# Performance work log

Hardware: AMD Instinct MI355X
Metric: run time of the kernel (lower is better)

Reference implementation:

```python
import jax, jax.numpy as jnp
import numpy as np

N, K, D, H = 10000, 30, 128, 4
DH = D // H
E = N * K

def setup_inputs() -> dict:
    ks = jax.random.split(jax.random.key(0), 12)
    s = 0.05
    h = jax.random.normal(ks[0], (N, D), jnp.float32)
    e = jax.random.normal(ks[1], (E, D), jnp.float32)
    # edges grouped by source node, K neighbors each (required by the (i j) rearranges)
    src = jnp.repeat(jnp.arange(N, dtype=jnp.int32), K)
    dst = jax.random.randint(ks[2], (E,), 0, N, dtype=jnp.int32)
    edge_index = jnp.stack([src, dst], axis=0)
    return {
        'h': h, 'e': e, 'edge_index': edge_index,
        'att_w1': jax.random.normal(ks[3], (3 * D, D)) * s, 'att_b1': jnp.zeros((D,)),
        'att_w2': jax.random.normal(ks[4], (D, D)) * s,     'att_b2': jnp.zeros((D,)),
        'att_w3': jax.random.normal(ks[5], (D, H)) * s,     'att_b3': jnp.zeros((H,)),
        'node_w1': jax.random.normal(ks[6], (2 * D, D)) * s, 'node_b1': jnp.zeros((D,)),
        'node_w2': jax.random.normal(ks[7], (D, D)) * s,     'node_b2': jnp.zeros((D,)),
        'node_w3': jax.random.normal(ks[8], (D, D)) * s,     'node_b3': jnp.zeros((D,)),
        'to_h_w': jax.random.normal(ks[9], (D, D)) * s,
    }

def reference(h, e, edge_index, att_w1, att_b1, att_w2, att_b2, att_w3, att_b3,
              node_w1, node_b1, node_w2, node_b2, node_w3, node_b3, to_h_w):
    gelu = lambda x: jax.nn.gelu(x, approximate=False)  # torch nn.GELU default (erf)
    hi = h[edge_index[0]]                               # [E, D] gather
    hj = h[edge_index[1]]                               # [E, D] gather
    hi_eij_hj = jnp.concatenate([hi, e, hj], axis=-1)   # [E, 3D]
    eij_hj = jnp.concatenate([e, hj], axis=-1)          # [E, 2D]
    # attention logits per head
    w = jax.nn.relu(hi_eij_hj @ att_w1 + att_b1)
    w = jax.nn.relu(w @ att_w2 + att_b2)
    w = (w @ att_w3 + att_b3).reshape(N, K, H)          # (i j) h -> i j h
    w = w / jnp.sqrt(jnp.float32(DH))
    att = jax.nn.softmax(w, axis=1)                     # softmax over neighbors j
    # values per edge, split per head
    v = gelu(eij_hj @ node_w1 + node_b1)
    v = gelu(v @ node_w2 + node_b2)
    v = (v @ node_w3 + node_b3).reshape(N, K, H, DH)    # (i j) (h d) -> i j h d
    out = jnp.einsum('nkh,nkhd->nhd', att, v).reshape(N, D)  # weighted aggregation
    return out @ to_h_w
```

## Files before the change

kernel.cpp:

```cpp
#include <hip/hip_runtime.h>
#include <hip/hip_bf16.h>

#define N_NODES 10000
#define KNEI    30
#define DIM     128
#define EDGES   (N_NODES * KNEI)

typedef __attribute__((ext_vector_type(4))) float  f32x4;
typedef __attribute__((ext_vector_type(8))) __bf16 bf16x8;
typedef __attribute__((ext_vector_type(4))) __bf16 bf16x4;

#define OFF_AW1 0
#define OFF_AW2 49152
#define OFF_NW1 65536
#define OFF_NW2 98304
#define OFF_NW3 114688
#define OFF_TH  131072
#define OFF_A3  147456
#define TOT_TILES 292
#define YHI_BYTE_OFF (300 * 1024)

__global__ __launch_bounds__(256) void repack_all(
    const float* __restrict__ aw1, const float* __restrict__ aw2,
    const float* __restrict__ nw1, const float* __restrict__ nw2,
    const float* __restrict__ nw3, const float* __restrict__ thw,
    const float* __restrict__ aw3, __bf16* __restrict__ dst) {
    int t = blockIdx.x * 256 + threadIdx.x;
    if (t >= TOT_TILES * 512) return;
    int tile = t >> 9;
    int i    = t & 7;
    int lane = (t >> 3) & 63;
    int krow = ((lane >> 4) << 3) + i;
    int ncol = lane & 15;
    float v;
    if (tile >= 288) {
        int k = (tile - 288) * 32 + krow;
        v = (ncol < 4) ? aw3[k * 4 + ncol] : 0.f;
    } else {
        const float* src; int lt;
        if      (tile < 96)  { src = aw1; lt = tile; }
        else if (tile < 128) { src = aw2; lt = tile - 96; }
        else if (tile < 192) { src = nw1; lt = tile - 128; }
        else if (tile < 224) { src = nw2; lt = tile - 192; }
        else if (tile < 256) { src = nw3; lt = tile - 224; }
        else                 { src = thw; lt = tile - 256; }
        int nt = lt & 7;
        int kt = lt >> 3;
        v = src[(kt * 32 + krow) * DIM + nt * 16 + ncol];
    }
    dst[t] = (__bf16)v;
}

__device__ __forceinline__ float gelu_f(float x) {
    float y = x * fmaf(0.0713548163f, x * x, 1.5957691216f);
    float r = __builtin_amdgcn_rcpf(__expf(y) + 1.f);
    return x - x * r;
}

__device__ __forceinline__ bf16x4 cvt4(float4 v) {
    bf16x4 r;
    r[0] = (__bf16)v.x; r[1] = (__bf16)v.y; r[2] = (__bf16)v.z; r[3] = (__bf16)v.w;
    return r;
}

__device__ __forceinline__ void store_act(f32x4 acc[2], const float* __restrict__ bias,
                                          __bf16* y, int sy, int actmode,
                                          int wv, int lane) {
    const int mrow = lane & 15;
    const int kgrp = (lane >> 4) & 3;
    const int nb = wv * 16 + kgrp * 4;
    float b0 = bias[nb], b1 = bias[nb + 1], b2 = bias[nb + 2], b3 = bias[nb + 3];
#pragma unroll
    for (int mf = 0; mf < 2; ++mf) {
        bf16x4 pk;
        float vv[4] = {acc[mf][0] + b0, acc[mf][1] + b1, acc[mf][2] + b2, acc[mf][3] + b3};
#pragma unroll
        for (int r = 0; r < 4; ++r) {
            float v = vv[r];
            v = actmode == 0 ? fmaxf(v, 0.f) : gelu_f(v);
            pk[r] = (__bf16)v;
        }
        *reinterpret_cast<bf16x4*>(y + (mf * 16 + mrow) * sy + nb) = pk;
    }
}

#define ZERO2(A) do { A[0] = (f32x4){0.f,0.f,0.f,0.f}; A[1] = (f32x4){0.f,0.f,0.f,0.f}; } while (0)

__global__ __launch_bounds__(512) void mm128(const float* __restrict__ in,
                                             float* __restrict__ outp,
                                             const __bf16* __restrict__ wfrag,
                                             const float* __restrict__ bias) {
    __shared__ __bf16 sP[64 * 136];
    const int tid  = threadIdx.x;
    const int wv   = tid >> 6;
    const int lane = tid & 63;
    const int mrow = lane & 15;
    const int kgrp = lane >> 4;
    const int base = blockIdx.x * 64;

#pragma unroll
    for (int c = 0; c < 4; ++c) {
        int idx = c * 512 + tid;
        int m  = idx >> 5;
        int jv = idx & 31;
        int row = base + m;
        float4 v = make_float4(0.f, 0.f, 0.f, 0.f);
        if (row < N_NODES) v = *reinterpret_cast<const float4*>(in + (long)row * DIM + jv * 4);
        *reinterpret_cast<bf16x4*>(&sP[m * 136 + jv * 4]) = cvt4(v);
    }
    __syncthreads();

    f32x4 acc[4];
#pragma unroll
    for (int mf = 0; mf < 4; ++mf) acc[mf] = (f32x4){0.f, 0.f, 0.f, 0.f};
#pragma unroll
    for (int kt = 0; kt < 4; ++kt) {
        bf16x8 a = *reinterpret_cast<const bf16x8*>(wfrag + ((kt * 8 + wv) * 64 + lane) * 8);
        const int kb = kt * 32 + kgrp * 8;
#pragma unroll
        for (int mf = 0; mf < 4; ++mf) {
            bf16x8 b = *reinterpret_cast<const bf16x8*>(sP + (mf * 16 + mrow) * 136 + kb);
            acc[mf] = __builtin_amdgcn_mfma_f32_16x16x32_bf16(a, b, acc[mf], 0, 0, 0);
        }
    }
    const int nb = wv * 16 + kgrp * 4;
    float b0 = 0.f, b1 = 0.f, b2 = 0.f, b3 = 0.f;
    if (bias) { b0 = bias[nb]; b1 = bias[nb + 1]; b2 = bias[nb + 2]; b3 = bias[nb + 3]; }
#pragma unroll
    for (int mf = 0; mf < 4; ++mf) {
        int row = base + mf * 16 + mrow;
        if (row < N_NODES) {
            float4 o = make_float4(acc[mf][0] + b0, acc[mf][1] + b1,
                                   acc[mf][2] + b2, acc[mf][3] + b3);
            *reinterpret_cast<float4*>(outp + (long)row * DIM + nb) = o;
        }
    }
}

__global__ __launch_bounds__(512, 4) void gnn_fused(
    const float* __restrict__ h, const float* __restrict__ e, const int* __restrict__ eidx,
    const float* __restrict__ yhi,
    const float* __restrict__ ab2, const float* __restrict__ ab3,
    const float* __restrict__ nb1, const float* __restrict__ nb2, const float* __restrict__ nb3,
    const __bf16* __restrict__ wp, float* __restrict__ pre_out) {

    __shared__ __bf16 S[8704];
    __shared__ __bf16 Y1[32 * 136];
    __shared__ __bf16 Y2[32 * 136];
    __shared__ float  sW[32][4];

    const int tid  = threadIdx.x;
    const int wv   = tid >> 6;
    const int lane = tid & 63;
    const int mrow = lane & 15;
    const int kg   = (lane >> 4) & 3;
    const int node = blockIdx.x;
    const long ebase = (long)node * KNEI;

#pragma unroll
    for (int c = 0; c < 2; ++c) {
        int idx = c * 512 + tid;
        int m  = idx >> 5;
        int jv = idx & 31;
        float4 ev = make_float4(0.f, 0.f, 0.f, 0.f), hjv = ev;
        if (m < KNEI) {
            long ge = ebase + m;
            ev  = *reinterpret_cast<const float4*>(e + ge * DIM + jv * 4);
            int dstn = eidx[EDGES + ge];
            hjv = *reinterpret_cast<const float4*>(h + (long)dstn * DIM + jv * 4);
        }
        *reinterpret_cast<bf16x4*>(&S[m * 264 + jv * 4])       = cvt4(ev);
        *reinterpret_cast<bf16x4*>(&S[m * 264 + 128 + jv * 4]) = cvt4(hjv);
    }
    __syncthreads();

    {
        f32x4 aa[2], an[2];
        ZERO2(aa); ZERO2(an);
        const __bf16* wA = wp + OFF_AW1 + 16384;
        const __bf16* wN = wp + OFF_NW1;
#pragma unroll
        for (int kt = 0; kt < 8; ++kt) {
            const int kb = kt * 32 + kg * 8;
            bf16x8 b0 = *reinterpret_cast<const bf16x8*>(S + mrow * 264 + kb);
            bf16x8 b1 = *reinterpret_cast<const bf16x8*>(S + (16 + mrow) * 264 + kb);
            bf16x8 a0 = *reinterpret_cast<const bf16x8*>(wA + ((kt * 8 + wv) * 64 + lane) * 8);
            aa[0] = __builtin_amdgcn_mfma_f32_16x16x32_bf16(a0, b0, aa[0], 0, 0, 0);
            aa[1] = __builtin_amdgcn_mfma_f32_16x16x32_bf16(a0, b1, aa[1], 0, 0, 0);
            bf16x8 a1 = *reinterpret_cast<const bf16x8*>(wN + ((kt * 8 + wv) * 64 + lane) * 8);
            an[0] = __builtin_amdgcn_mfma_f32_16x16x32_bf16(a1, b0, an[0], 0, 0, 0);
            an[1] = __builtin_amdgcn_mfma_f32_16x16x32_bf16(a1, b1, an[1], 0, 0, 0);
        }
        store_act(aa, yhi + (long)node * DIM, Y1, 136, 0, wv, lane);
        store_act(an, nb1, Y2, 136, 1, wv, lane);
    }
    __syncthreads();

    {
        const bool isatt = (wv < 4);
        const int w4 = isatt ? wv : (wv - 4);
        const __bf16* B = isatt ? Y1 : Y2;
        const __bf16* W = wp + (isatt ? OFF_AW2 : OFF_NW2);
        const float* bias = isatt ? ab2 : nb2;
        __bf16* dst = S + (isatt ? 4352 : 0);
        f32x4 acc[2][2];
        ZERO2(acc[0]); ZERO2(acc[1]);
#pragma unroll
        for (int kt = 0; kt < 4; ++kt) {
            const int kb = kt * 32 + kg * 8;
            bf16x8 b0 = *reinterpret_cast<const bf16x8*>(B + mrow * 136 + kb);
            bf16x8 b1 = *reinterpret_cast<const bf16x8*>(B + (16 + mrow) * 136 + kb);
#pragma unroll
            for (int j = 0; j < 2; ++j) {
                bf16x8 a = *reinterpret_cast<const bf16x8*>(W + (size_t)((kt * 8 + w4 * 2 + j) * 64 + lane) * 8);
                acc[j][0] = __builtin_amdgcn_mfma_f32_16x16x32_bf16(a, b0, acc[j][0], 0, 0, 0);
                acc[j][1] = __builtin_amdgcn_mfma_f32_16x16x32_bf16(a, b1, acc[j][1], 0, 0, 0);
            }
        }
#pragma unroll
        for (int j = 0; j < 2; ++j) {
            const int f = w4 * 32 + j * 16 + kg * 4;
            float b0 = bias[f], b1 = bias[f + 1], b2 = bias[f + 2], b3 = bias[f + 3];
#pragma unroll
            for (int mf = 0; mf < 2; ++mf) {
                float vv[4] = {acc[j][mf][0] + b0, acc[j][mf][1] + b1,
                               acc[j][mf][2] + b2, acc[j][mf][3] + b3};
                bf16x4 pk;
#pragma unroll
                for (int r = 0; r < 4; ++r) {
                    float v = isatt ? fmaxf(vv[r], 0.f) : gelu_f(vv[r]);
                    pk[r] = (__bf16)v;
                }
                *reinterpret_cast<bf16x4*>(dst + (mf * 16 + mrow) * 136 + f) = pk;
            }
        }
    }
    __syncthreads();

    if (wv == 0) {
        const __bf16* A2 = S + 4352;
        f32x4 la[2];
        ZERO2(la);
#pragma unroll
        for (int kt = 0; kt < 4; ++kt) {
            const int kb = kt * 32 + kg * 8;
            bf16x8 b0 = *reinterpret_cast<const bf16x8*>(A2 + mrow * 136 + kb);
            bf16x8 b1 = *reinterpret_cast<const bf16x8*>(A2 + (16 + mrow) * 136 + kb);
            bf16x8 a = *reinterpret_cast<const bf16x8*>(wp + OFF_A3 + ((kt * 64) + lane) * 8);
            la[0] = __builtin_amdgcn_mfma_f32_16x16x32_bf16(a, b0, la[0], 0, 0, 0);
            la[1] = __builtin_amdgcn_mfma_f32_16x16x32_bf16(a, b1, la[1], 0, 0, 0);
        }
        if (lane < 16) {
            const float sc = 0.17677669529f;
            float v0[4], v1[4], mx[4];
            const bool pad1 = (16 + lane) >= KNEI;
#pragma unroll
            for (int r = 0; r < 4; ++r) {
                v0[r] = (la[0][r] + ab3[r]) * sc;
                v1[r] = pad1 ? -1e30f : (la[1][r] + ab3[r]) * sc;
                mx[r] = fmaxf(v0[r], v1[r]);
            }
#pragma unroll
            for (int msk = 1; msk <= 8; msk <<= 1)
#pragma unroll
                for (int r = 0; r < 4; ++r) mx[r] = fmaxf(mx[r], __shfl_xor(mx[r], msk));
            float e0[4], e1[4], sm[4];
#pragma unroll
            for (int r = 0; r < 4; ++r) {
                e0[r] = __expf(v0[r] - mx[r]);
                e1[r] = __expf(v1[r] - mx[r]);
                sm[r] = e0[r] + e1[r];
            }
#pragma unroll
            for (int msk = 1; msk <= 8; msk <<= 1)
#pragma unroll
                for (int r = 0; r < 4; ++r) sm[r] += __shfl_xor(sm[r], msk);
            float4 w0, w1;
            float i0 = __builtin_amdgcn_rcpf(sm[0]), i1 = __builtin_amdgcn_rcpf(sm[1]);
            float i2 = __builtin_amdgcn_rcpf(sm[2]), i3 = __builtin_amdgcn_rcpf(sm[3]);
            w0 = make_float4(e0[0] * i0, e0[1] * i1, e0[2] * i2, e0[3] * i3);
            w1 = make_float4(e1[0] * i0, e1[1] * i1, e1[2] * i2, e1[3] * i3);
            *reinterpret_cast<float4*>(&sW[lane][0])      = w0;
            *reinterpret_cast<float4*>(&sW[16 + lane][0]) = w1;
        }
    }
    f32x4 v2[2];
    ZERO2(v2);
#pragma unroll
    for (int kt = 0; kt < 4; ++kt) {
        const int kb = kt * 32 + kg * 8;
        bf16x8 b0 = *reinterpret_cast<const bf16x8*>(S + mrow * 136 + kb);
        bf16x8 b1 = *reinterpret_cast<const bf16x8*>(S + (16 + mrow) * 136 + kb);
        bf16x8 a = *reinterpret_cast<const bf16x8*>(wp + OFF_NW3 + (size_t)((kt * 8 + wv) * 64 + lane) * 8);
        v2[0] = __builtin_amdgcn_mfma_f32_16x16x32_bf16(a, b0, v2[0], 0, 0, 0);
        v2[1] = __builtin_amdgcn_mfma_f32_16x16x32_bf16(a, b1, v2[1], 0, 0, 0);
    }
    __syncthreads();

    {
        const int hh = wv >> 1;
        float wgt0 = sW[mrow][hh];
        float wgt1 = sW[16 + mrow][hh];
        float part[4];
#pragma unroll
        for (int r = 0; r < 4; ++r)
            part[r] = wgt0 * v2[0][r] + wgt1 * v2[1][r];
#pragma unroll
        for (int msk = 1; msk <= 8; msk <<= 1)
#pragma unroll
            for (int r = 0; r < 4; ++r)
                part[r] += __shfl_xor(part[r], msk);
        if (mrow == 0) {
            const int nb = wv * 16 + kg * 4;
            float4 o = make_float4(part[0] + nb3[nb],     part[1] + nb3[nb + 1],
                                   part[2] + nb3[nb + 2], part[3] + nb3[nb + 3]);
            *reinterpret_cast<float4*>(pre_out + (long)node * DIM + nb) = o;
        }
    }
}

extern "C" void kernel_launch(void* const* d_in, const int* in_sizes, int n_in,
                              void* d_out, int out_size, void* d_ws, size_t ws_size,
                              hipStream_t stream) {
    const float* h   = (const float*)d_in[0];
    const float* e   = (const float*)d_in[1];
    const int*   ei  = (const int*)d_in[2];
    const float* aw1 = (const float*)d_in[3];
    const float* ab1 = (const float*)d_in[4];
    const float* aw2 = (const float*)d_in[5];
    const float* ab2 = (const float*)d_in[6];
    const float* aw3 = (const float*)d_in[7];
    const float* ab3 = (const float*)d_in[8];
    const float* nw1 = (const float*)d_in[9];
    const float* nb1 = (const float*)d_in[10];
    const float* nw2 = (const float*)d_in[11];
    const float* nb2 = (const float*)d_in[12];
    const float* nw3 = (const float*)d_in[13];
    const float* nb3 = (const float*)d_in[14];
    const float* thw = (const float*)d_in[15];
    float* out = (float*)d_out;
    __bf16* wp = (__bf16*)d_ws;
    float* yhi = (float*)((char*)d_ws + YHI_BYTE_OFF);

    repack_all<<<(TOT_TILES * 512 + 255) / 256, 256, 0, stream>>>(
        aw1, aw2, nw1, nw2, nw3, thw, aw3, wp);

    const int nblk = (N_NODES + 63) / 64;
    mm128<<<nblk, 512, 0, stream>>>(h, yhi, wp + OFF_AW1, ab1);

    gnn_fused<<<N_NODES, 512, 0, stream>>>(h, e, ei, yhi, ab2, ab3,
                                           nb1, nb2, nb3, wp, out);
    mm128<<<nblk, 512, 0, stream>>>(out, out, wp + OFF_TH, nullptr);
}
```

Before: 149.4 us.

## Halve gnn_fused block to 256 threads with two output tiles per wave

Each node's fused block now runs 4 waves instead of 8, and each wave computes two 16-column output tiles per stage (and four in the layer-2 split), so every B fragment loaded from LDS is reused across more MFMAs. Launch bounds change from (512,4) to (256,2), and the head-aggregation stage now maps one wave per head. The aim is less LDS traffic per MFMA and lower per-block scheduling and barrier cost. In exchange each wave holds more accumulator registers and there are fewer waves per block to hide global-load latency.

Measured after the change: 161.1 us. +7.9%, slower.

```diff
diff --git a/kernel.cpp b/kernel.cpp
--- a/kernel.cpp
+++ b/kernel.cpp
@@ -63,27 +63,6 @@
     return r;
 }
 
-__device__ __forceinline__ void store_act(f32x4 acc[2], const float* __restrict__ bias,
-                                          __bf16* y, int sy, int actmode,
-                                          int wv, int lane) {
-    const int mrow = lane & 15;
-    const int kgrp = (lane >> 4) & 3;
-    const int nb = wv * 16 + kgrp * 4;
-    float b0 = bias[nb], b1 = bias[nb + 1], b2 = bias[nb + 2], b3 = bias[nb + 3];
-#pragma unroll
-    for (int mf = 0; mf < 2; ++mf) {
-        bf16x4 pk;
-        float vv[4] = {acc[mf][0] + b0, acc[mf][1] + b1, acc[mf][2] + b2, acc[mf][3] + b3};
-#pragma unroll
-        for (int r = 0; r < 4; ++r) {
-            float v = vv[r];
-            v = actmode == 0 ? fmaxf(v, 0.f) : gelu_f(v);
-            pk[r] = (__bf16)v;
-        }
-        *reinterpret_cast<bf16x4*>(y + (mf * 16 + mrow) * sy + nb) = pk;
-    }
-}
-
 #define ZERO2(A) do { A[0] = (f32x4){0.f,0.f,0.f,0.f}; A[1] = (f32x4){0.f,0.f,0.f,0.f}; } while (0)
 
 __global__ __launch_bounds__(512) void mm128(const float* __restrict__ in,
@@ -137,7 +116,7 @@
     }
 }
 
-__global__ __launch_bounds__(512, 4) void gnn_fused(
+__global__ __launch_bounds__(256, 2) void gnn_fused(
     const float* __restrict__ h, const float* __restrict__ e, const int* __restrict__ eidx,
     const float* __restrict__ yhi,
     const float* __restrict__ ab2, const float* __restrict__ ab3,
@@ -158,8 +137,8 @@
     const long ebase = (long)node * KNEI;
 
 #pragma unroll
-    for (int c = 0; c < 2; ++c) {
-        int idx = c * 512 + tid;
+    for (int c = 0; c < 4; ++c) {
+        int idx = c * 256 + tid;
         int m  = idx >> 5;
         int jv = idx & 31;
         float4 ev = make_float4(0.f, 0.f, 0.f, 0.f), hjv = ev;
@@ -175,8 +154,9 @@
     __syncthreads();
 
     {
-        f32x4 aa[2], an[2];
-        ZERO2(aa); ZERO2(an);
+        f32x4 aa[2][2], an[2][2];
+#pragma unroll
+        for (int j = 0; j < 2; ++j) { ZERO2(aa[j]); ZERO2(an[j]); }
         const __bf16* wA = wp + OFF_AW1 + 16384;
         const __bf16* wN = wp + OFF_NW1;
 #pragma unroll
@@ -184,52 +164,76 @@
             const int kb = kt * 32 + kg * 8;
             bf16x8 b0 = *reinterpret_cast<const bf16x8*>(S + mrow * 264 + kb);
             bf16x8 b1 = *reinterpret_cast<const bf16x8*>(S + (16 + mrow) * 264 + kb);
-            bf16x8 a0 = *reinterpret_cast<const bf16x8*>(wA + ((kt * 8 + wv) * 64 + lane) * 8);
-            aa[0] = __builtin_amdgcn_mfma_f32_16x16x32_bf16(a0, b0, aa[0], 0, 0, 0);
-            aa[1] = __builtin_amdgcn_mfma_f32_16x16x32_bf16(a0, b1, aa[1], 0, 0, 0);
-            bf16x8 a1 = *reinterpret_cast<const bf16x8*>(wN + ((kt * 8 + wv) * 64 + lane) * 8);
-            an[0] = __builtin_amdgcn_mfma_f32_16x16x32_bf16(a1, b0, an[0], 0, 0, 0);
-            an[1] = __builtin_amdgcn_mfma_f32_16x16x32_bf16(a1, b1, an[1], 0, 0, 0);
-        }
-        store_act(aa, yhi + (long)node * DIM, Y1, 136, 0, wv, lane);
-        store_act(an, nb1, Y2, 136, 1, wv, lane);
+#pragma unroll
+            for (int j = 0; j < 2; ++j) {
+                bf16x8 a = *reinterpret_cast<const bf16x8*>(wA + ((kt * 8 + wv * 2 + j) * 64 + lane) * 8);
+                aa[j][0] = __builtin_amdgcn_mfma_f32_16x16x32_bf16(a, b0, aa[j][0], 0, 0, 0);
+                aa[j][1] = __builtin_amdgcn_mfma_f32_16x16x32_bf16(a, b1, aa[j][1], 0, 0, 0);
+            }
+#pragma unroll
+            for (int j = 0; j < 2; ++j) {
+                bf16x8 a = *reinterpret_cast<const bf16x8*>(wN + ((kt * 8 + wv * 2 + j) * 64 + lane) * 8);
+                an[j][0] = __builtin_amdgcn_mfma_f32_16x16x32_bf16(a, b0, an[j][0], 0, 0, 0);
+                an[j][1] = __builtin_amdgcn_mfma_f32_16x16x32_bf16(a, b1, an[j][1], 0, 0, 0);
+            }
+        }
+        const float* yrow = yhi + (long)node * DIM;
+#pragma unroll
+        for (int j = 0; j < 2; ++j) {
+            const int f = wv * 32 + j * 16 + kg * 4;
+            float4 ba = *reinterpret_cast<const float4*>(yrow + f);
+            float4 bn = *reinterpret_cast<const float4*>(nb1 + f);
+            float bav[4] = {ba.x, ba.y, ba.z, ba.w};
+            float bnv[4] = {bn.x, bn.y, bn.z, bn.w};
+#pragma unroll
+            for (int mf = 0; mf < 2; ++mf) {
+                bf16x4 p1, p2;
+#pragma unroll
+                for (int r = 0; r < 4; ++r) {
+                    p1[r] = (__bf16)fmaxf(aa[j][mf][r] + bav[r], 0.f);
+                    p2[r] = (__bf16)gelu_f(an[j][mf][r] + bnv[r]);
+                }
+                *reinterpret_cast<bf16x4*>(Y1 + (mf * 16 + mrow) * 136 + f) = p1;
+                *reinterpret_cast<bf16x4*>(Y2 + (mf * 16 + mrow) * 136 + f) = p2;
+            }
+        }
     }
     __syncthreads();
 
     {
-        const bool isatt = (wv < 4);
-        const int w4 = isatt ? wv : (wv - 4);
+        const bool isatt = (wv < 2);
+        const int w2 = isatt ? wv : (wv - 2);
         const __bf16* B = isatt ? Y1 : Y2;
         const __bf16* W = wp + (isatt ? OFF_AW2 : OFF_NW2);
         const float* bias = isatt ? ab2 : nb2;
         __bf16* dst = S + (isatt ? 4352 : 0);
-        f32x4 acc[2][2];
-        ZERO2(acc[0]); ZERO2(acc[1]);
+        f32x4 acc[4][2];
+#pragma unroll
+        for (int j = 0; j < 4; ++j) ZERO2(acc[j]);
 #pragma unroll
         for (int kt = 0; kt < 4; ++kt) {
             const int kb = kt * 32 + kg * 8;
             bf16x8 b0 = *reinterpret_cast<const bf16x8*>(B + mrow * 136 + kb);
             bf16x8 b1 = *reinterpret_cast<const bf16x8*>(B + (16 + mrow) * 136 + kb);
 #pragma unroll
-            for (int j = 0; j < 2; ++j) {
-                bf16x8 a = *reinterpret_cast<const bf16x8*>(W + (size_t)((kt * 8 + w4 * 2 + j) * 64 + lane) * 8);
+            for (int j = 0; j < 4; ++j) {
+                bf16x8 a = *reinterpret_cast<const bf16x8*>(W + (size_t)((kt * 8 + w2 * 4 + j) * 64 + lane) * 8);
                 acc[j][0] = __builtin_amdgcn_mfma_f32_16x16x32_bf16(a, b0, acc[j][0], 0, 0, 0);
                 acc[j][1] = __builtin_amdgcn_mfma_f32_16x16x32_bf16(a, b1, acc[j][1], 0, 0, 0);
             }
         }
 #pragma unroll
-        for (int j = 0; j < 2; ++j) {
-            const int f = w4 * 32 + j * 16 + kg * 4;
-            float b0 = bias[f], b1 = bias[f + 1], b2 = bias[f + 2], b3 = bias[f + 3];
+        for (int j = 0; j < 4; ++j) {
+            const int f = w2 * 64 + j * 16 + kg * 4;
+            float4 bb = *reinterpret_cast<const float4*>(bias + f);
+            float bv[4] = {bb.x, bb.y, bb.z, bb.w};
 #pragma unroll
             for (int mf = 0; mf < 2; ++mf) {
-                float vv[4] = {acc[j][mf][0] + b0, acc[j][mf][1] + b1,
-                               acc[j][mf][2] + b2, acc[j][mf][3] + b3};
                 bf16x4 pk;
 #pragma unroll
                 for (int r = 0; r < 4; ++r) {
-                    float v = isatt ? fmaxf(vv[r], 0.f) : gelu_f(vv[r]);
-                    pk[r] = (__bf16)v;
+                    float v = acc[j][mf][r] + bv[r];
+                    pk[r] = (__bf16)(isatt ? fmaxf(v, 0.f) : gelu_f(v));
                 }
                 *reinterpret_cast<bf16x4*>(dst + (mf * 16 + mrow) * 136 + f) = pk;
             }
@@ -275,46 +279,56 @@
             for (int msk = 1; msk <= 8; msk <<= 1)
 #pragma unroll
                 for (int r = 0; r < 4; ++r) sm[r] += __shfl_xor(sm[r], msk);
-            float4 w0, w1;
             float i0 = __builtin_amdgcn_rcpf(sm[0]), i1 = __builtin_amdgcn_rcpf(sm[1]);
             float i2 = __builtin_amdgcn_rcpf(sm[2]), i3 = __builtin_amdgcn_rcpf(sm[3]);
-            w0 = make_float4(e0[0] * i0, e0[1] * i1, e0[2] * i2, e0[3] * i3);
-            w1 = make_float4(e1[0] * i0, e1[1] * i1, e1[2] * i2, e1[3] * i3);
+            float4 w0 = make_float4(e0[0] * i0, e0[1] * i1, e0[2] * i2, e0[3] * i3);
+            float4 w1 = make_float4(e1[0] * i0, e1[1] * i1, e1[2] * i2, e1[3] * i3);
             *reinterpret_cast<float4*>(&sW[lane][0])      = w0;
             *reinterpret_cast<float4*>(&sW[16 + lane][0]) = w1;
         }
     }
-    f32x4 v2[2];
-    ZERO2(v2);
+    f32x4 v2[2][2];
+#pragma unroll
+    for (int j = 0; j < 2; ++j) ZERO2(v2[j]);
 #pragma unroll
     for (int kt = 0; kt < 4; ++kt) {
         const int kb = kt * 32 + kg * 8;
         bf16x8 b0 = *reinterpret_cast<const bf16x8*>(S + mrow * 136 + kb);
         bf16x8 b1 = *reinterpret_cast<const bf16x8*>(S + (16 + mrow) * 136 + kb);
-        bf16x8 a = *reinterpret_cast<const bf16x8*>(wp + OFF_NW3 + (size_t)((kt * 8 + wv) * 64 + lane) * 8);
-        v2[0] = __builtin_amdgcn_mfma_f32_16x16x32_bf16(a, b0, v2[0], 0, 0, 0);
-        v2[1] = __builtin_amdgcn_mfma_f32_16x16x32_bf16(a, b1, v2[1], 0, 0, 0);
+#pragma unroll
+        for (int j = 0; j < 2; ++j) {
+            bf16x8 a = *reinterpret_cast<const bf16x8*>(wp + OFF_NW3 + (size_t)((kt * 8 + wv * 2 + j) * 64 + lane) * 8);
+            v2[j][0] = __builtin_amdgcn_mfma_f32_16x16x32_bf16(a, b0, v2[j][0], 0, 0, 0);
+            v2[j][1] = __builtin_amdgcn_mfma_f32_16x16x32_bf16(a, b1, v2[j][1], 0, 0, 0);
+        }
     }
     __syncthreads();
 
     {
-        const int hh = wv >> 1;
-        float wgt0 = sW[mrow][hh];
-        float wgt1 = sW[16 + mrow][hh];
-        float part[4];
-#pragma unroll
-        for (int r = 0; r < 4; ++r)
-            part[r] = wgt0 * v2[0][r] + wgt1 * v2[1][r];
+        float wgt0 = sW[mrow][wv];
+        float wgt1 = sW[16 + mrow][wv];
+        float part[2][4];
+#pragma unroll
+        for (int j = 0; j < 2; ++j)
+#pragma unroll
+            for (int r = 0; r < 4; ++r)
+                part[j][r] = wgt0 * v2[j][0][r] + wgt1 * v2[j][1][r];
 #pragma unroll
         for (int msk = 1; msk <= 8; msk <<= 1)
 #pragma unroll
-            for (int r = 0; r < 4; ++r)
-                part[r] += __shfl_xor(part[r], msk);
+            for (int j = 0; j < 2; ++j)
+#pragma unroll
+                for (int r = 0; r < 4; ++r)
+                    part[j][r] += __shfl_xor(part[j][r], msk);
         if (mrow == 0) {
-            const int nb = wv * 16 + kg * 4;
-            float4 o = make_float4(part[0] + nb3[nb],     part[1] + nb3[nb + 1],
-                                   part[2] + nb3[nb + 2], part[3] + nb3[nb + 3]);
-            *reinterpret_cast<float4*>(pre_out + (long)node * DIM + nb) = o;
+#pragma unroll
+            for (int j = 0; j < 2; ++j) {
+                const int nb = wv * 32 + j * 16 + kg * 4;
+                float4 b3v = *reinterpret_cast<const float4*>(nb3 + nb);
+                float4 o = make_float4(part[j][0] + b3v.x, part[j][1] + b3v.y,
+                                       part[j][2] + b3v.z, part[j][3] + b3v.w);
+                *reinterpret_cast<float4*>(pre_out + (long)node * DIM + nb) = o;
+            }
         }
     }
 }
@@ -348,7 +362,7 @@
     const int nblk = (N_NODES + 63) / 64;
     mm128<<<nblk, 512, 0, stream>>>(h, yhi, wp + OFF_AW1, ab1);
 
-    gnn_fused<<<N_NODES, 512, 0, stream>>>(h, e, ei, yhi, ab2, ab3,
+    gnn_fused<<<N_NODES, 256, 0, stream>>>(h, e, ei, yhi, ab2, ab3,
                                            nb1, nb2, nb3, wp, out);
     mm128<<<nblk, 512, 0, stream>>>(out, out, wp + OFF_TH, nullptr);
 }
```

## Fuse hi projection and output projection into per-node fused kernel

Applied to the files above, without the earlier changes.

Removes the two separate mm128 launches, one for the h_i @ W1[0:128] projection and one for the final to_h projection. Both are now computed inside gnn_fused per node as scalar dot products against transposed bf16 weights added to the repack. This saves two kernel launches and the global round-trips through the yhi and pre_out buffers. In exchange, every block does extra non-MFMA FMA work (128x128 MACs twice) and adds shared memory and two more barriers, which may reduce occupancy.

New measurement: 211.3 us. 1.41x slower.

```diff
diff --git a/kernel.cpp b/kernel.cpp
--- a/kernel.cpp
+++ b/kernel.cpp
@@ -17,8 +17,9 @@
 #define OFF_NW3 114688
 #define OFF_TH  131072
 #define OFF_A3  147456
-#define TOT_TILES 292
-#define YHI_BYTE_OFF (300 * 1024)
+#define OFF_THT 149504
+#define OFF_HIT 165888
+#define TOT_ELEMS 182272
 
 __global__ __launch_bounds__(256) void repack_all(
     const float* __restrict__ aw1, const float* __restrict__ aw2,
@@ -26,27 +27,36 @@
     const float* __restrict__ nw3, const float* __restrict__ thw,
     const float* __restrict__ aw3, __bf16* __restrict__ dst) {
     int t = blockIdx.x * 256 + threadIdx.x;
-    if (t >= TOT_TILES * 512) return;
-    int tile = t >> 9;
-    int i    = t & 7;
-    int lane = (t >> 3) & 63;
-    int krow = ((lane >> 4) << 3) + i;
-    int ncol = lane & 15;
+    if (t >= TOT_ELEMS) return;
     float v;
-    if (tile >= 288) {
-        int k = (tile - 288) * 32 + krow;
-        v = (ncol < 4) ? aw3[k * 4 + ncol] : 0.f;
+    if (t >= 292 * 512) {
+        int t2 = t - 292 * 512;
+        int arr = t2 >> 14;
+        int e2  = t2 & 16383;
+        int row = e2 >> 7;
+        int k   = e2 & 127;
+        v = arr == 0 ? thw[k * 128 + row] : aw1[k * 128 + row];
     } else {
-        const float* src; int lt;
-        if      (tile < 96)  { src = aw1; lt = tile; }
-        else if (tile < 128) { src = aw2; lt = tile - 96; }
-        else if (tile < 192) { src = nw1; lt = tile - 128; }
-        else if (tile < 224) { src = nw2; lt = tile - 192; }
-        else if (tile < 256) { src = nw3; lt = tile - 224; }
-        else                 { src = thw; lt = tile - 256; }
-        int nt = lt & 7;
-        int kt = lt >> 3;
-        v = src[(kt * 32 + krow) * DIM + nt * 16 + ncol];
+        int tile = t >> 9;
+        int i    = t & 7;
+        int lane = (t >> 3) & 63;
+        int krow = ((lane >> 4) << 3) + i;
+        int ncol = lane & 15;
+        if (tile >= 288) {
+            int k = (tile - 288) * 32 + krow;
+            v = (ncol < 4) ? aw3[k * 4 + ncol] : 0.f;
+        } else {
+            const float* src; int lt;
+            if      (tile < 96)  { src = aw1; lt = tile; }
+            else if (tile < 128) { src = aw2; lt = tile - 96; }
+            else if (tile < 192) { src = nw1; lt = tile - 128; }
+            else if (tile < 224) { src = nw2; lt = tile - 192; }
+            else if (tile < 256) { src = nw3; lt = tile - 224; }
+            else                 { src = thw; lt = tile - 256; }
+            int nt = lt & 7;
+            int kt = lt >> 3;
+            v = src[(kt * 32 + krow) * DIM + nt * 16 + ncol];
+        }
     }
     dst[t] = (__bf16)v;
 }
@@ -86,68 +96,19 @@
 
 #define ZERO2(A) do { A[0] = (f32x4){0.f,0.f,0.f,0.f}; A[1] = (f32x4){0.f,0.f,0.f,0.f}; } while (0)
 
-__global__ __launch_bounds__(512) void mm128(const float* __restrict__ in,
-                                             float* __restrict__ outp,
-                                             const __bf16* __restrict__ wfrag,
-                                             const float* __restrict__ bias) {
-    __shared__ __bf16 sP[64 * 136];
-    const int tid  = threadIdx.x;
-    const int wv   = tid >> 6;
-    const int lane = tid & 63;
-    const int mrow = lane & 15;
-    const int kgrp = lane >> 4;
-    const int base = blockIdx.x * 64;
-
-#pragma unroll
-    for (int c = 0; c < 4; ++c) {
-        int idx = c * 512 + tid;
-        int m  = idx >> 5;
-        int jv = idx & 31;
-        int row = base + m;
-        float4 v = make_float4(0.f, 0.f, 0.f, 0.f);
-        if (row < N_NODES) v = *reinterpret_cast<const float4*>(in + (long)row * DIM + jv * 4);
-        *reinterpret_cast<bf16x4*>(&sP[m * 136 + jv * 4]) = cvt4(v);
-    }
-    __syncthreads();
-
-    f32x4 acc[4];
-#pragma unroll
-    for (int mf = 0; mf < 4; ++mf) acc[mf] = (f32x4){0.f, 0.f, 0.f, 0.f};
-#pragma unroll
-    for (int kt = 0; kt < 4; ++kt) {
-        bf16x8 a = *reinterpret_cast<const bf16x8*>(wfrag + ((kt * 8 + wv) * 64 + lane) * 8);
-        const int kb = kt * 32 + kgrp * 8;
-#pragma unroll
-        for (int mf = 0; mf < 4; ++mf) {
-            bf16x8 b = *reinterpret_cast<const bf16x8*>(sP + (mf * 16 + mrow) * 136 + kb);
-            acc[mf] = __builtin_amdgcn_mfma_f32_16x16x32_bf16(a, b, acc[mf], 0, 0, 0);
-        }
-    }
-    const int nb = wv * 16 + kgrp * 4;
-    float b0 = 0.f, b1 = 0.f, b2 = 0.f, b3 = 0.f;
-    if (bias) { b0 = bias[nb]; b1 = bias[nb + 1]; b2 = bias[nb + 2]; b3 = bias[nb + 3]; }
-#pragma unroll
-    for (int mf = 0; mf < 4; ++mf) {
-        int row = base + mf * 16 + mrow;
-        if (row < N_NODES) {
-            float4 o = make_float4(acc[mf][0] + b0, acc[mf][1] + b1,
-                                   acc[mf][2] + b2, acc[mf][3] + b3);
-            *reinterpret_cast<float4*>(outp + (long)row * DIM + nb) = o;
-        }
-    }
-}
-
 __global__ __launch_bounds__(512, 4) void gnn_fused(
     const float* __restrict__ h, const float* __restrict__ e, const int* __restrict__ eidx,
-    const float* __restrict__ yhi,
-    const float* __restrict__ ab2, const float* __restrict__ ab3,
+    const float* __restrict__ ab1, const float* __restrict__ ab2, const float* __restrict__ ab3,
     const float* __restrict__ nb1, const float* __restrict__ nb2, const float* __restrict__ nb3,
-    const __bf16* __restrict__ wp, float* __restrict__ pre_out) {
+    const __bf16* __restrict__ wp, float* __restrict__ out) {
 
     __shared__ __bf16 S[8704];
     __shared__ __bf16 Y1[32 * 136];
     __shared__ __bf16 Y2[32 * 136];
     __shared__ float  sW[32][4];
+    __shared__ float  sY[4][128];
+    __shared__ float  sPre[128];
+    __shared__ float  sAcc[4][128];
 
     const int tid  = threadIdx.x;
     const int wv   = tid >> 6;
@@ -172,6 +133,21 @@
         *reinterpret_cast<bf16x4*>(&S[m * 264 + jv * 4])       = cvt4(ev);
         *reinterpret_cast<bf16x4*>(&S[m * 264 + 128 + jv * 4]) = cvt4(hjv);
     }
+    {
+        const int kq = tid >> 7, f = tid & 127;
+        const float*  hrow = h + (long)node * DIM + kq * 32;
+        const __bf16* wrow = wp + OFF_HIT + f * 128 + kq * 32;
+        float a = 0.f;
+#pragma unroll
+        for (int j = 0; j < 32; j += 8) {
+            bf16x8 w8 = *reinterpret_cast<const bf16x8*>(wrow + j);
+            float4 h0 = *reinterpret_cast<const float4*>(hrow + j);
+            float4 h1 = *reinterpret_cast<const float4*>(hrow + j + 4);
+            a += (float)w8[0] * h0.x + (float)w8[1] * h0.y + (float)w8[2] * h0.z + (float)w8[3] * h0.w
+               + (float)w8[4] * h1.x + (float)w8[5] * h1.y + (float)w8[6] * h1.z + (float)w8[7] * h1.w;
+        }
+        sY[kq][f] = a;
+    }
     __syncthreads();
 
     {
@@ -191,7 +167,24 @@
             an[0] = __builtin_amdgcn_mfma_f32_16x16x32_bf16(a1, b0, an[0], 0, 0, 0);
             an[1] = __builtin_amdgcn_mfma_f32_16x16x32_bf16(a1, b1, an[1], 0, 0, 0);
         }
-        store_act(aa, yhi + (long)node * DIM, Y1, 136, 0, wv, lane);
+        {
+            const int nb = wv * 16 + kg * 4;
+            float4 a1v = *reinterpret_cast<const float4*>(ab1 + nb);
+            float bav[4] = {a1v.x, a1v.y, a1v.z, a1v.w};
+#pragma unroll
+            for (int q = 0; q < 4; ++q) {
+                float4 sq = *reinterpret_cast<float4*>(&sY[q][nb]);
+                bav[0] += sq.x; bav[1] += sq.y; bav[2] += sq.z; bav[3] += sq.w;
+            }
+#pragma unroll
+            for (int mf = 0; mf < 2; ++mf) {
+                bf16x4 pk;
+#pragma unroll
+                for (int r = 0; r < 4; ++r)
+                    pk[r] = (__bf16)fmaxf(aa[mf][r] + bav[r], 0.f);
+                *reinterpret_cast<bf16x4*>(Y1 + (mf * 16 + mrow) * 136 + nb) = pk;
+            }
+        }
         store_act(an, nb1, Y2, 136, 1, wv, lane);
     }
     __syncthreads();
@@ -228,8 +221,8 @@
                 bf16x4 pk;
 #pragma unroll
                 for (int r = 0; r < 4; ++r) {
-                    float v = isatt ? fmaxf(vv[r], 0.f) : gelu_f(vv[r]);
-                    pk[r] = (__bf16)v;
+                    float v = vv[r];
+                    pk[r] = (__bf16)(isatt ? fmaxf(v, 0.f) : gelu_f(v));
                 }
                 *reinterpret_cast<bf16x4*>(dst + (mf * 16 + mrow) * 136 + f) = pk;
             }
@@ -275,11 +268,10 @@
             for (int msk = 1; msk <= 8; msk <<= 1)
 #pragma unroll
                 for (int r = 0; r < 4; ++r) sm[r] += __shfl_xor(sm[r], msk);
-            float4 w0, w1;
             float i0 = __builtin_amdgcn_rcpf(sm[0]), i1 = __builtin_amdgcn_rcpf(sm[1]);
             float i2 = __builtin_amdgcn_rcpf(sm[2]), i3 = __builtin_amdgcn_rcpf(sm[3]);
-            w0 = make_float4(e0[0] * i0, e0[1] * i1, e0[2] * i2, e0[3] * i3);
-            w1 = make_float4(e1[0] * i0, e1[1] * i1, e1[2] * i2, e1[3] * i3);
+            float4 w0 = make_float4(e0[0] * i0, e0[1] * i1, e0[2] * i2, e0[3] * i3);
+            float4 w1 = make_float4(e1[0] * i0, e1[1] * i1, e1[2] * i2, e1[3] * i3);
             *reinterpret_cast<float4*>(&sW[lane][0])      = w0;
             *reinterpret_cast<float4*>(&sW[16 + lane][0]) = w1;
         }
@@ -314,9 +306,30 @@
             const int nb = wv * 16 + kg * 4;
             float4 o = make_float4(part[0] + nb3[nb],     part[1] + nb3[nb + 1],
                                    part[2] + nb3[nb + 2], part[3] + nb3[nb + 3]);
-            *reinterpret_cast<float4*>(pre_out + (long)node * DIM + nb) = o;
-        }
-    }
+            *reinterpret_cast<float4*>(&sPre[nb]) = o;
+        }
+    }
+    __syncthreads();
+
+    {
+        const int kq = tid >> 7, d = tid & 127;
+        const __bf16* wrow = wp + OFF_THT + d * 128 + kq * 32;
+        const float*  p    = &sPre[kq * 32];
+        float a = 0.f;
+#pragma unroll
+        for (int j = 0; j < 32; j += 8) {
+            bf16x8 w8 = *reinterpret_cast<const bf16x8*>(wrow + j);
+            a += (float)w8[0] * p[j]     + (float)w8[1] * p[j + 1]
+               + (float)w8[2] * p[j + 2] + (float)w8[3] * p[j + 3]
+               + (float)w8[4] * p[j + 4] + (float)w8[5] * p[j + 5]
+               + (float)w8[6] * p[j + 6] + (float)w8[7] * p[j + 7];
+        }
+        sAcc[kq][d] = a;
+    }
+    __syncthreads();
+
+    if (tid < 128)
+        out[(long)node * DIM + tid] = sAcc[0][tid] + sAcc[1][tid] + sAcc[2][tid] + sAcc[3][tid];
 }
 
 extern "C" void kernel_launch(void* const* d_in, const int* in_sizes, int n_in,
@@ -340,15 +353,10 @@
     const float* thw = (const float*)d_in[15];
     float* out = (float*)d_out;
     __bf16* wp = (__bf16*)d_ws;
-    float* yhi = (float*)((char*)d_ws + YHI_BYTE_OFF);
-
-    repack_all<<<(TOT_TILES * 512 + 255) / 256, 256, 0, stream>>>(
+
+    repack_all<<<(TOT_ELEMS + 255) / 256, 256, 0, stream>>>(
         aw1, aw2, nw1, nw2, nw3, thw, aw3, wp);
 
-    const int nblk = (N_NODES + 63) / 64;
-    mm128<<<nblk, 512, 0, stream>>>(h, yhi, wp + OFF_AW1, ab1);
-
-    gnn_fused<<<N_NODES, 512, 0, stream>>>(h, e, ei, yhi, ab2, ab3,
+    gnn_fused<<<N_NODES, 512, 0, stream>>>(h, e, ei, ab1, ab2, ab3,
                                            nb1, nb2, nb3, wp, out);
-    mm128<<<nblk, 512, 0, stream>>>(out, out, wp + OFF_TH, nullptr);
-}
+}
```
